# Optimization experiments

Hardware: AMD Instinct MI355X
Metric: run time of the kernel (lower is better)

Reference implementation:

```python
import jax, jax.numpy as jnp
import numpy as np

N_OBJ, N_REL = 16384, 32768
HID, POOL = 512, 4096
N_OBJ_CLS, N_REL_CLS = 151, 51


def setup_inputs() -> dict:
    key = jax.random.key(0)
    ks = jax.random.split(key, 12)
    return {
        "edge_ctx": jax.random.normal(ks[0], (N_OBJ, HID), jnp.float32),
        "union_features": jax.random.normal(ks[1], (N_REL, POOL), jnp.float32),
        "pair_idx": jax.random.randint(ks[2], (N_REL, 2), 0, N_OBJ, jnp.int64) if jax.config.jax_enable_x64 else jax.random.randint(ks[2], (N_REL, 2), 0, N_OBJ, jnp.int32),
        "obj_preds": jax.random.randint(ks[3], (N_OBJ,), 0, N_OBJ_CLS, jnp.int32),
        "W_post_emb": jax.random.normal(ks[4], (2 * HID, HID), jnp.float32) * (10.0 / np.sqrt(HID)),
        "b_post_emb": jax.random.normal(ks[5], (2 * HID,), jnp.float32) * 0.01,
        "W_post_cat": jax.random.normal(ks[6], (POOL, 2 * HID), jnp.float32) * (1.0 / np.sqrt(2 * HID)),
        "b_post_cat": jax.random.normal(ks[7], (POOL,), jnp.float32) * 0.01,
        "W_rel": jax.random.normal(ks[8], (N_REL_CLS, POOL), jnp.float32) * (1.0 / np.sqrt(POOL)),
        "b_rel": jax.random.normal(ks[9], (N_REL_CLS,), jnp.float32) * 0.01,
        "freq_bias": jax.random.normal(ks[10], (N_OBJ_CLS, N_OBJ_CLS, N_REL_CLS), jnp.float32),
    }


def reference(edge_ctx, union_features, pair_idx, obj_preds,
              W_post_emb, b_post_emb, W_post_cat, b_post_cat,
              W_rel, b_rel, freq_bias):
    # post_emb: [N_obj, H] -> [N_obj, 2H] -> head/tail reps [N_obj, H]
    edge_rep = edge_ctx @ W_post_emb.T + b_post_emb            # [N_obj, 2H]
    edge_rep = edge_rep.reshape(edge_rep.shape[0], 2, HID)
    head_rep = edge_rep[:, 0]                                  # [N_obj, H]
    tail_rep = edge_rep[:, 1]                                  # [N_obj, H]

    h_idx = pair_idx[:, 0]
    t_idx = pair_idx[:, 1]
    # gather + concat head/tail pair features -> [N_rel, 2H]
    prod_rep = jnp.concatenate([head_rep[h_idx], tail_rep[t_idx]], axis=-1)
    # post_cat linear -> [N_rel, POOL]
    prod_rep = prod_rep @ W_post_cat.T + b_post_cat
    # use_vision, pooling_dim == MLP_HEAD_DIM -> elementwise product
    prod_rep = prod_rep * union_features
    # rel_compress -> [N_rel, num_rel_cls]
    rel_dists = prod_rep @ W_rel.T + b_rel
    # frequency bias lookup indexed by (head class, tail class)
    bias = freq_bias[obj_preds[h_idx], obj_preds[t_idx]]       # [N_rel, num_rel_cls]
    return rel_dists + bias
```

## Files before the change

### kernel.cpp

```cpp
#include <hip/hip_runtime.h>

#define N_OBJ 16384
#define N_REL 32768
#define HID 512
#define POOL 4096
#define NCLS 151
#define NRELCLS 51

#define AS1 __attribute__((address_space(1)))
#define AS3 __attribute__((address_space(3)))

#define LDSSZ 131072

typedef __attribute__((ext_vector_type(8))) short short8;
typedef __attribute__((ext_vector_type(4))) float f32x4;

__device__ __forceinline__ unsigned short f2bf(float x) {
    unsigned u = __float_as_uint(x);
    u += 0x7fff + ((u >> 16) & 1);
    return (unsigned short)(u >> 16);
}

__global__ void cvt_kernel(const float* __restrict__ in, unsigned short* __restrict__ out, long n8) {
    long i = (long)blockIdx.x * blockDim.x + threadIdx.x;
    if (i >= n8) return;
    const float4* p = (const float4*)in;
    float4 a = p[2 * i], b = p[2 * i + 1];
    short8 o;
    o[0] = f2bf(a.x); o[1] = f2bf(a.y); o[2] = f2bf(a.z); o[3] = f2bf(a.w);
    o[4] = f2bf(b.x); o[5] = f2bf(b.y); o[6] = f2bf(b.z); o[7] = f2bf(b.w);
    ((short8*)out)[i] = o;
}

__global__ void cvt_wrel_kernel(const float* __restrict__ W, unsigned short* __restrict__ out) {
    int gid = blockIdx.x * 256 + threadIdx.x;
    int row = gid >> 9;
    int c8 = (gid & 511) << 3;
    short8 o = {};
    if (row < NRELCLS) {
        const float* src = W + (long)row * POOL + c8;
        float4 a = *(const float4*)src, b = *(const float4*)(src + 4);
        o[0] = f2bf(a.x); o[1] = f2bf(a.y); o[2] = f2bf(a.z); o[3] = f2bf(a.w);
        o[4] = f2bf(b.x); o[5] = f2bf(b.y); o[6] = f2bf(b.z); o[7] = f2bf(b.w);
    }
    *(short8*)(out + (long)row * POOL + c8) = o;
}

__device__ __forceinline__ void stage_tile128x64(const unsigned short* __restrict__ src,
                                                 unsigned short* lds,
                                                 int row0, int rowStrideElems, int col0,
                                                 int wave, int lane) {
    const char* s = (const char*)(src + (long)row0 * rowStrideElems + col0);
    long strideB = (long)rowStrideElems * 2;
#pragma unroll
    for (int is = 0; is < 4; ++is) {
        int issue = wave * 4 + is;
        const char* g = s + (long)(issue * 8 + (lane >> 3)) * strideB + (lane & 7) * 16;
        __builtin_amdgcn_global_load_lds((const AS1 void*)g,
                                         (AS3 void*)((char*)lds + issue * 1024),
                                         16, 0, 0);
    }
}

__global__ __launch_bounds__(256) void gemm1_kernel(const unsigned short* __restrict__ A,
                                                    const unsigned short* __restrict__ B,
                                                    const float* __restrict__ bias,
                                                    unsigned short* __restrict__ C) {
    __shared__ __align__(16) unsigned short At[128 * 64];
    __shared__ __align__(16) unsigned short Bt[128 * 64];
    int row0 = blockIdx.x * 128, col0 = blockIdx.y * 128;
    int tid = threadIdx.x, wave = tid >> 6, lane = tid & 63;
    int wr = (wave >> 1) * 64, wc = (wave & 1) * 64;
    int lrow = lane & 15, lko = (lane >> 4) * 8;
    f32x4 acc[4][4] = {};
    for (int kt = 0; kt < HID / 64; ++kt) {
        stage_tile128x64(A, At, row0, HID, kt * 64, wave, lane);
        stage_tile128x64(B, Bt, col0, HID, kt * 64, wave, lane);
        __syncthreads();
#pragma unroll
        for (int ks = 0; ks < 2; ++ks) {
            short8 af[4], bf[4];
#pragma unroll
            for (int mi = 0; mi < 4; ++mi) af[mi] = *(const short8*)(At + (wr + 16 * mi + lrow) * 64 + ks * 32 + lko);
#pragma unroll
            for (int ni = 0; ni < 4; ++ni) bf[ni] = *(const short8*)(Bt + (wc + 16 * ni + lrow) * 64 + ks * 32 + lko);
#pragma unroll
            for (int mi = 0; mi < 4; ++mi)
#pragma unroll
                for (int ni = 0; ni < 4; ++ni)
                    acc[mi][ni] = __builtin_amdgcn_mfma_f32_16x16x32_bf16(af[mi], bf[ni], acc[mi][ni], 0, 0, 0);
        }
        __syncthreads();
    }
#pragma unroll
    for (int mi = 0; mi < 4; ++mi)
#pragma unroll
        for (int ni = 0; ni < 4; ++ni)
#pragma unroll
            for (int i = 0; i < 4; ++i) {
                int r = row0 + wr + 16 * mi + 4 * (lane >> 4) + i;
                int c = col0 + wc + 16 * ni + lrow;
                C[(long)r * 1024 + c] = f2bf(acc[mi][ni][i] + bias[c]);
            }
}

__global__ void gather_kernel(const unsigned short* __restrict__ edge_rep,
                              const int* __restrict__ pair_idx,
                              unsigned short* __restrict__ A2) {
    long gid = (long)blockIdx.x * 256 + threadIdx.x;
    int r = (int)(gid >> 7), j = (int)(gid & 127);
    int src = (j < 64) ? pair_idx[2 * r] : pair_idx[2 * r + 1];
    const uint4* s = (const uint4*)(edge_rep + (long)src * 1024);
    ((uint4*)(A2 + (long)r * 1024))[j] = s[j];
}

__global__ void init_out_kernel(const int* __restrict__ pair_idx, const int* __restrict__ obj_preds,
                                const float* __restrict__ b_rel, const float* __restrict__ freq_bias,
                                float* __restrict__ out) {
    int r = blockIdx.x * 4 + (threadIdx.x >> 6);
    int lane = threadIdx.x & 63;
    if (lane < NRELCLS) {
        int h = pair_idx[2 * r], t = pair_idx[2 * r + 1];
        long idx = ((long)obj_preds[h] * NCLS + obj_preds[t]) * NRELCLS + lane;
        out[(long)r * NRELCLS + lane] = b_rel[lane] + freq_bias[idx];
    }
}

__device__ __forceinline__ void stage_ab(const char* __restrict__ A2b, const char* __restrict__ Wcb,
                                         char* lds, int s, int t, int row0, int col0,
                                         int w, int lane) {
    int kb = t * 64;
#pragma unroll
    for (int i = 0; i < 2; ++i) {
        int obase = i * 8192 + w * 1024;
        int o = obase + lane * 16;
        int row = o >> 6, cin = o & 63;
        int c = cin ^ ((row & 3) << 4);
        __builtin_amdgcn_global_load_lds((const AS1 void*)(A2b + (long)(row0 + row) * 2048 + kb + c),
                                         (AS3 void*)(lds + s * 16384 + obase), 16, 0, 0);
        __builtin_amdgcn_global_load_lds((const AS1 void*)(Wcb + (long)(col0 + row) * 2048 + kb + c),
                                         (AS3 void*)(lds + 65536 + s * 16384 + obase), 16, 0, 0);
    }
}

__device__ __forceinline__ void kstep(const char* lds, int s, int wr, int wc, int lrow, int lcb,
                                      f32x4 acc[8][4]) {
    const char* A = lds + s * 16384;
    const char* B = lds + 65536 + s * 16384;
    short8 bfr[4];
#pragma unroll
    for (int ni = 0; ni < 4; ++ni) {
        int r = wc + 16 * ni + lrow;
        bfr[ni] = *(const short8*)(B + r * 64 + (lcb ^ ((r & 3) << 4)));
    }
    __builtin_amdgcn_s_setprio(1);
#pragma unroll
    for (int mi = 0; mi < 8; ++mi) {
        int r = wr + 16 * mi + lrow;
        short8 a = *(const short8*)(A + r * 64 + (lcb ^ ((r & 3) << 4)));
#pragma unroll
        for (int ni = 0; ni < 4; ++ni)
            acc[mi][ni] = __builtin_amdgcn_mfma_f32_16x16x32_bf16(a, bfr[ni], acc[mi][ni], 0, 0, 0);
    }
    __builtin_amdgcn_s_setprio(0);
}

__global__ __launch_bounds__(512, 1) void fused_kernel(
    const unsigned short* __restrict__ A2,
    const unsigned short* __restrict__ Wcat,
    const unsigned short* __restrict__ Wrelp,
    const float* __restrict__ unionf,
    const float* __restrict__ bcat,
    float* __restrict__ out) {
    __shared__ __align__(16) char lds[LDSSZ];
    int row0 = blockIdx.x * 256, col0 = blockIdx.y * 256;
    int tid = threadIdx.x, w = tid >> 6, lane = tid & 63;
    int wr = (w >> 2) * 128, wc = (w & 3) * 64;
    int lrow = lane & 15, lcb = (lane >> 4) * 16;
    const char* A2b = (const char*)A2;
    const char* Wcb = (const char*)Wcat;
    f32x4 acc2[8][4] = {};

    stage_ab(A2b, Wcb, lds, 0, 0, row0, col0, w, lane);
    stage_ab(A2b, Wcb, lds, 1, 1, row0, col0, w, lane);
    stage_ab(A2b, Wcb, lds, 2, 2, row0, col0, w, lane);

    for (int t = 0; t < 30; ++t) {
        asm volatile("s_waitcnt vmcnt(8)" ::: "memory");
        __builtin_amdgcn_s_barrier();
        __builtin_amdgcn_sched_barrier(0);
        if (t < 29) stage_ab(A2b, Wcb, lds, (t + 3) & 3, t + 3, row0, col0, w, lane);
        kstep(lds, t & 3, wr, wc, lrow, lcb, acc2);
    }
    asm volatile("s_waitcnt vmcnt(4)" ::: "memory");
    __builtin_amdgcn_s_barrier();
    __builtin_amdgcn_sched_barrier(0);
    kstep(lds, 30 & 3, wr, wc, lrow, lcb, acc2);
    asm volatile("s_waitcnt vmcnt(0)" ::: "memory");
    __builtin_amdgcn_s_barrier();
    __builtin_amdgcn_sched_barrier(0);
    kstep(lds, 31 & 3, wr, wc, lrow, lcb, acc2);

    asm volatile("s_waitcnt lgkmcnt(0)" ::: "memory");
    __builtin_amdgcn_sched_barrier(0);
    __builtin_amdgcn_s_barrier();
    __builtin_amdgcn_sched_barrier(0);

    {
        float bcv[4];
#pragma unroll
        for (int ni = 0; ni < 4; ++ni) bcv[ni] = bcat[col0 + wc + 16 * ni + lrow];
#pragma unroll
        for (int mi = 0; mi < 8; ++mi)
#pragma unroll
            for (int ni = 0; ni < 4; ++ni) {
                int pcol = wc + 16 * ni + lrow;
#pragma unroll
                for (int i = 0; i < 4; ++i) {
                    int prow = wr + 16 * mi + 4 * (lane >> 4) + i;
                    float u = __builtin_nontemporal_load(
                        &unionf[(long)(row0 + prow) * 4096 + col0 + pcol]);
                    *(unsigned short*)(lds + prow * 512 + ((pcol * 2) ^ ((prow & 7) << 4)))
                        = f2bf((acc2[mi][ni][i] + bcv[ni]) * u);
                }
            }
    }
    asm volatile("s_waitcnt lgkmcnt(0)" ::: "memory");
    __builtin_amdgcn_sched_barrier(0);
    __builtin_amdgcn_s_barrier();
    __builtin_amdgcn_sched_barrier(0);

    f32x4 acc3[2][4] = {};
    const char* Wrb = (const char*)Wrelp;
#pragma unroll
    for (int ks = 0; ks < 8; ++ks) {
        int cb2 = ks * 64 + lcb;
        short8 wb[4], pa[2];
#pragma unroll
        for (int ni = 0; ni < 4; ++ni) {
            int r2 = 16 * ni + lrow;
            wb[ni] = *(const short8*)(Wrb + (long)r2 * 8192 + col0 * 2 + cb2);
        }
#pragma unroll
        for (int mi = 0; mi < 2; ++mi) {
            int r2 = w * 32 + 16 * mi + lrow;
            pa[mi] = *(const short8*)(lds + r2 * 512 + (cb2 ^ ((r2 & 7) << 4)));
        }
#pragma unroll
        for (int mi = 0; mi < 2; ++mi)
#pragma unroll
            for (int ni = 0; ni < 4; ++ni)
                acc3[mi][ni] = __builtin_amdgcn_mfma_f32_16x16x32_bf16(pa[mi], wb[ni], acc3[mi][ni], 0, 0, 0);
    }
#pragma unroll
    for (int mi = 0; mi < 2; ++mi)
#pragma unroll
        for (int ni = 0; ni < 4; ++ni)
#pragma unroll
            for (int i = 0; i < 4; ++i) {
                int r = row0 + w * 32 + 16 * mi + 4 * (lane >> 4) + i;
                int cc = 16 * ni + lrow;
                if (cc < NRELCLS) atomicAdd(out + (long)r * NRELCLS + cc, acc3[mi][ni][i]);
            }
}

extern "C" void kernel_launch(void* const* d_in, const int* in_sizes, int n_in,
                              void* d_out, int out_size, void* d_ws, size_t ws_size,
                              hipStream_t stream) {
    const float* edge_ctx  = (const float*)d_in[0];
    const float* unionf    = (const float*)d_in[1];
    const int*   pair_idx  = (const int*)d_in[2];
    const int*   obj_preds = (const int*)d_in[3];
    const float* W_emb     = (const float*)d_in[4];
    const float* b_emb     = (const float*)d_in[5];
    const float* W_cat     = (const float*)d_in[6];
    const float* b_cat     = (const float*)d_in[7];
    const float* W_rel     = (const float*)d_in[8];
    const float* b_rel     = (const float*)d_in[9];
    const float* freq_bias = (const float*)d_in[10];
    float* out = (float*)d_out;

    char* ws = (char*)d_ws;
    unsigned short* ecb   = (unsigned short*)ws; ws += (size_t)N_OBJ * HID * 2;
    unsigned short* Wembb = (unsigned short*)ws; ws += (size_t)1024 * HID * 2;
    unsigned short* Wcatb = (unsigned short*)ws; ws += (size_t)POOL * 1024 * 2;
    unsigned short* Wrelb = (unsigned short*)ws; ws += (size_t)64 * POOL * 2;
    unsigned short* erep  = (unsigned short*)ws; ws += (size_t)N_OBJ * 1024 * 2;
    unsigned short* A2    = (unsigned short*)ws; ws += (size_t)N_REL * 1024 * 2;

    cvt_kernel<<<4096, 256, 0, stream>>>(edge_ctx, ecb, (long)N_OBJ * HID / 8);
    cvt_kernel<<<256, 256, 0, stream>>>(W_emb, Wembb, (long)1024 * HID / 8);
    cvt_kernel<<<2048, 256, 0, stream>>>(W_cat, Wcatb, (long)POOL * 1024 / 8);
    cvt_wrel_kernel<<<128, 256, 0, stream>>>(W_rel, Wrelb);
    gemm1_kernel<<<dim3(128, 8), 256, 0, stream>>>(ecb, Wembb, b_emb, erep);
    gather_kernel<<<16384, 256, 0, stream>>>(erep, pair_idx, A2);
    init_out_kernel<<<8192, 256, 0, stream>>>(pair_idx, obj_preds, b_rel, freq_bias, out);
    fused_kernel<<<dim3(128, 16), 512, 0, stream>>>(A2, Wcatb, Wrelb, unionf, b_cat, out);
}
```

Measured before the change: 581.2 us.

## Fuse pair gather into GEMM A-tile loads and remap blocks per XCD

Removes the separate gather kernel and the materialized A2 buffer. The fused GEMM now loads head/tail rows of erep directly into LDS using per-thread pair indices. The grid becomes 1D with a mapping that places each pair of column panels on one XCD to improve L2 reuse of W_cat. This trades coalesced A-tile loads for indexed row loads.

```diff
diff --git a/kernel.cpp b/kernel.cpp
--- a/kernel.cpp
+++ b/kernel.cpp
@@ -104,16 +104,6 @@
             }
 }
 
-__global__ void gather_kernel(const unsigned short* __restrict__ edge_rep,
-                              const int* __restrict__ pair_idx,
-                              unsigned short* __restrict__ A2) {
-    long gid = (long)blockIdx.x * 256 + threadIdx.x;
-    int r = (int)(gid >> 7), j = (int)(gid & 127);
-    int src = (j < 64) ? pair_idx[2 * r] : pair_idx[2 * r + 1];
-    const uint4* s = (const uint4*)(edge_rep + (long)src * 1024);
-    ((uint4*)(A2 + (long)r * 1024))[j] = s[j];
-}
-
 __global__ void init_out_kernel(const int* __restrict__ pair_idx, const int* __restrict__ obj_preds,
                                 const float* __restrict__ b_rel, const float* __restrict__ freq_bias,
                                 float* __restrict__ out) {
@@ -126,20 +116,21 @@
     }
 }
 
-__device__ __forceinline__ void stage_ab(const char* __restrict__ A2b, const char* __restrict__ Wcb,
-                                         char* lds, int s, int t, int row0, int col0,
-                                         int w, int lane) {
+__device__ __forceinline__ void stage_ab(const char* __restrict__ erepb, const char* __restrict__ Wcb,
+                                         char* lds, int s, int t, int col0,
+                                         const int* hA, const int* tA, const int* colbA,
+                                         const int* obaseA, int w, int lane) {
     int kb = t * 64;
 #pragma unroll
     for (int i = 0; i < 2; ++i) {
-        int obase = i * 8192 + w * 1024;
-        int o = obase + lane * 16;
+        int idx = (kb < 1024) ? hA[i] : tA[i];
+        __builtin_amdgcn_global_load_lds((const AS1 void*)(erepb + (long)idx * 2048 + kb + colbA[i]),
+                                         (AS3 void*)(lds + s * 16384 + obaseA[i]), 16, 0, 0);
+        int o = obaseA[i] + lane * 16;
         int row = o >> 6, cin = o & 63;
         int c = cin ^ ((row & 3) << 4);
-        __builtin_amdgcn_global_load_lds((const AS1 void*)(A2b + (long)(row0 + row) * 2048 + kb + c),
-                                         (AS3 void*)(lds + s * 16384 + obase), 16, 0, 0);
         __builtin_amdgcn_global_load_lds((const AS1 void*)(Wcb + (long)(col0 + row) * 2048 + kb + c),
-                                         (AS3 void*)(lds + 65536 + s * 16384 + obase), 16, 0, 0);
+                                         (AS3 void*)(lds + 65536 + s * 16384 + obaseA[i]), 16, 0, 0);
     }
 }
 
@@ -166,30 +157,45 @@
 }
 
 __global__ __launch_bounds__(512, 1) void fused_kernel(
-    const unsigned short* __restrict__ A2,
+    const unsigned short* __restrict__ erep,
     const unsigned short* __restrict__ Wcat,
     const unsigned short* __restrict__ Wrelp,
     const float* __restrict__ unionf,
     const float* __restrict__ bcat,
+    const int* __restrict__ pair_idx,
     float* __restrict__ out) {
     __shared__ __align__(16) char lds[LDSSZ];
-    int row0 = blockIdx.x * 256, col0 = blockIdx.y * 256;
+    int bid = blockIdx.x;
+    int xcd = bid & 7, j = bid >> 3;
+    int panel = (xcd << 1) | (j >> 7);
+    int row0 = (j & 127) * 256, col0 = panel * 256;
     int tid = threadIdx.x, w = tid >> 6, lane = tid & 63;
     int wr = (w >> 2) * 128, wc = (w & 3) * 64;
     int lrow = lane & 15, lcb = (lane >> 4) * 16;
-    const char* A2b = (const char*)A2;
+    const char* erepb = (const char*)erep;
     const char* Wcb = (const char*)Wcat;
     f32x4 acc2[8][4] = {};
 
-    stage_ab(A2b, Wcb, lds, 0, 0, row0, col0, w, lane);
-    stage_ab(A2b, Wcb, lds, 1, 1, row0, col0, w, lane);
-    stage_ab(A2b, Wcb, lds, 2, 2, row0, col0, w, lane);
+    int hA[2], tA[2], colbA[2], obaseA[2];
+#pragma unroll
+    for (int i = 0; i < 2; ++i) {
+        obaseA[i] = i * 8192 + w * 1024;
+        int o = obaseA[i] + lane * 16;
+        int arow = o >> 6, cin = o & 63;
+        colbA[i] = cin ^ ((arow & 3) << 4);
+        hA[i] = pair_idx[2 * (row0 + arow)];
+        tA[i] = pair_idx[2 * (row0 + arow) + 1];
+    }
+
+    stage_ab(erepb, Wcb, lds, 0, 0, col0, hA, tA, colbA, obaseA, w, lane);
+    stage_ab(erepb, Wcb, lds, 1, 1, col0, hA, tA, colbA, obaseA, w, lane);
+    stage_ab(erepb, Wcb, lds, 2, 2, col0, hA, tA, colbA, obaseA, w, lane);
 
     for (int t = 0; t < 30; ++t) {
         asm volatile("s_waitcnt vmcnt(8)" ::: "memory");
         __builtin_amdgcn_s_barrier();
         __builtin_amdgcn_sched_barrier(0);
-        if (t < 29) stage_ab(A2b, Wcb, lds, (t + 3) & 3, t + 3, row0, col0, w, lane);
+        if (t < 29) stage_ab(erepb, Wcb, lds, (t + 3) & 3, t + 3, col0, hA, tA, colbA, obaseA, w, lane);
         kstep(lds, t & 3, wr, wc, lrow, lcb, acc2);
     }
     asm volatile("s_waitcnt vmcnt(4)" ::: "memory");
@@ -286,14 +292,12 @@
     unsigned short* Wcatb = (unsigned short*)ws; ws += (size_t)POOL * 1024 * 2;
     unsigned short* Wrelb = (unsigned short*)ws; ws += (size_t)64 * POOL * 2;
     unsigned short* erep  = (unsigned short*)ws; ws += (size_t)N_OBJ * 1024 * 2;
-    unsigned short* A2    = (unsigned short*)ws; ws += (size_t)N_REL * 1024 * 2;
 
     cvt_kernel<<<4096, 256, 0, stream>>>(edge_ctx, ecb, (long)N_OBJ * HID / 8);
     cvt_kernel<<<256, 256, 0, stream>>>(W_emb, Wembb, (long)1024 * HID / 8);
     cvt_kernel<<<2048, 256, 0, stream>>>(W_cat, Wcatb, (long)POOL * 1024 / 8);
     cvt_wrel_kernel<<<128, 256, 0, stream>>>(W_rel, Wrelb);
     gemm1_kernel<<<dim3(128, 8), 256, 0, stream>>>(ecb, Wembb, b_emb, erep);
-    gather_kernel<<<16384, 256, 0, stream>>>(erep, pair_idx, A2);
     init_out_kernel<<<8192, 256, 0, stream>>>(pair_idx, obj_preds, b_rel, freq_bias, out);
-    fused_kernel<<<dim3(128, 16), 512, 0, stream>>>(A2, Wcatb, Wrelb, unionf, b_cat, out);
-}
+    fused_kernel<<<2048, 512, 0, stream>>>(erep, Wcatb, Wrelb, unionf, b_cat, pair_idx, out);
+}
```

Measured after the change: 552.0 us. -5.0%, faster.
